# Optimization experiments

Measured on AMD Instinct MI355X. Metric: run time of the kernel, lower is better.

Reference implementation:

```python
import jax, jax.numpy as jnp
import numpy as np

N = 100000      # nodes
E = 1600000     # edges
H = 128         # hidden_channels
G = 128         # graphs in batch
L = 3           # num_layers
C = 4           # num_classes
BN_EPS = 1e-5


def setup_inputs() -> dict:
    key = jax.random.key(0)
    ks = jax.random.split(key, 24)
    s = 0.05
    x = jax.random.randint(ks[0], (N, 3), 0, 5, dtype=jnp.int64)
    edge_index = jax.random.randint(ks[1], (2, E), 0, N, dtype=jnp.int64)
    batch = jnp.sort(jax.random.randint(ks[2], (N,), 0, G, dtype=jnp.int64))
    p = lambda k, shp: jax.random.normal(k, shp, dtype=jnp.float32) * s
    return {
        'x': x, 'edge_index': edge_index, 'batch': batch,
        'node_emb': p(ks[3], (5, H)),
        'comp_emb': p(ks[4], (6, H)),
        'pin_emb':  p(ks[5], (6, H)),
        'proj_w': p(ks[6], (3 * H, H)), 'proj_b': p(ks[7], (H,)),
        'gin_w1': p(ks[8], (L, H, 2 * H)), 'gin_b1': p(ks[9], (L, 2 * H)),
        'gin_w2': p(ks[10], (L, 2 * H, H)), 'gin_b2': p(ks[11], (L, H)),
        'bn_gamma': jnp.ones((L, H), jnp.float32),
        'bn_beta': jnp.zeros((L, H), jnp.float32),
        'fus_w1': p(ks[12], (3 * H, 2 * H)), 'fus_b1': p(ks[13], (2 * H,)),
        'fus_w2': p(ks[14], (2 * H, H)), 'fus_b2': p(ks[15], (H,)),
        'cls_w': p(ks[16], (H, C)), 'cls_b': p(ks[17], (C,)),
    }


def _encoder(x, edge_index, batch, node_emb, comp_emb, pin_emb, proj_w, proj_b,
             gin_w1, gin_b1, gin_w2, gin_b2, bn_gamma, bn_beta):
    # embedding concat + projection
    idx = jnp.clip(x, 0, None)
    h = jnp.concatenate([node_emb[idx[:, 0]], comp_emb[idx[:, 1]], pin_emb[idx[:, 2]]], axis=1)
    h = h @ proj_w + proj_b                      # [N, H]
    src, dst = edge_index[0], edge_index[1]
    for i in range(L):
        # GINConv (eps=0): MLP(x + sum_{j->i} x_j)
        agg = jax.ops.segment_sum(h[src], dst, num_segments=N)
        z = h + agg
        z = jax.nn.relu(z @ gin_w1[i] + gin_b1[i]) @ gin_w2[i] + gin_b2[i]
        # BatchNorm1d (training-mode batch statistics), ReLU, residual
        mu = jnp.mean(z, axis=0)
        var = jnp.mean((z - mu) ** 2, axis=0)
        z = (z - mu) * jax.lax.rsqrt(var + BN_EPS) * bn_gamma[i] + bn_beta[i]
        z = jax.nn.relu(z)
        if i > 0:
            z = z + h
        h = z  # dropout = identity (eval)
    # global mean / max / sum pooling
    counts = jax.ops.segment_sum(jnp.ones((N,), h.dtype), batch, num_segments=G)
    gsum = jax.ops.segment_sum(h, batch, num_segments=G)
    gmean = gsum / jnp.maximum(counts, 1.0)[:, None]
    gmax = jax.ops.segment_max(h, batch, num_segments=G)
    gmax = jnp.where(jnp.isfinite(gmax), gmax, 0.0)
    return jnp.concatenate([gmean, gmax, gsum], axis=1)  # [G, 3H]


def reference(x, edge_index, batch, node_emb, comp_emb, pin_emb, proj_w, proj_b,
              gin_w1, gin_b1, gin_w2, gin_b2, bn_gamma, bn_beta,
              fus_w1, fus_b1, fus_w2, fus_b2, cls_w, cls_b):
    emb = _encoder(x, edge_index, batch, node_emb, comp_emb, pin_emb, proj_w, proj_b,
                   gin_w1, gin_b1, gin_w2, gin_b2, bn_gamma, bn_beta)
    f = jax.nn.relu(emb @ fus_w1 + fus_b1)
    f = jax.nn.relu(f @ fus_w2 + fus_b2)
    return f @ cls_w + cls_b                     # [G, C] logits
```

## Files before the change

kernel.cpp:

```cpp
#include <hip/hip_runtime.h>
#include <hip/hip_bf16.h>


#define NN 100000
#define NE 1600000
#define HD 128
#define NG 128
#define NL 3
#define BN_EPS 1e-5f
#define MPAD 100096
#define PCH 8

typedef unsigned short u16;
typedef __attribute__((ext_vector_type(8))) short short8v;
typedef __attribute__((ext_vector_type(4))) float f32x4;

__device__ inline u16 bf16_hi(float v) {
    __hip_bfloat16 h = __float2bfloat16(v);
    return *(u16*)&h;
}
__device__ inline float bf16_f(u16 u) {
    __hip_bfloat16 h = *(__hip_bfloat16*)&u;
    return __bfloat162float(h);
}
__device__ inline void split_bf16(float v, u16* hi, u16* lo) {
    u16 h = bf16_hi(v);
    *hi = h;
    *lo = bf16_hi(v - bf16_f(h));
}

__device__ inline void gload_lds16(const void* g, void* l) {
    __builtin_amdgcn_global_load_lds(
        (const __attribute__((address_space(1))) void*)g,
        (__attribute__((address_space(3))) void*)l, 16, 0, 0);
}

__global__ void proj_tables_kernel(const float* __restrict__ node_emb,
                                   const float* __restrict__ comp_emb,
                                   const float* __restrict__ pin_emb,
                                   const float* __restrict__ proj_w,
                                   float* __restrict__ P) {
    int c = threadIdx.x;
    for (int r = 0; r < 17; ++r) {
        const float* emb;
        int base;
        if (r < 5)        { emb = node_emb + r * HD;        base = 0; }
        else if (r < 11)  { emb = comp_emb + (r - 5) * HD;  base = HD; }
        else              { emb = pin_emb + (r - 11) * HD;  base = 2 * HD; }
        float acc = 0.f;
        for (int k = 0; k < HD; ++k)
            acc += emb[k] * proj_w[(size_t)(base + k) * HD + c];
        P[r * HD + c] = acc;
    }
}

__global__ __launch_bounds__(256) void embed_kernel(const int* __restrict__ x,
                                                    const float* __restrict__ P,
                                                    const float* __restrict__ proj_b,
                                                    float* __restrict__ h) {
    int i = blockIdx.x * 256 + threadIdx.x;
    int n = i >> 5;
    if (n >= NN) return;
    int c4 = (i & 31) * 4;
    int i0 = x[3 * n + 0]; i0 = i0 < 0 ? 0 : (i0 > 4 ? 4 : i0);
    int i1 = x[3 * n + 1]; i1 = i1 < 0 ? 0 : (i1 > 5 ? 5 : i1);
    int i2 = x[3 * n + 2]; i2 = i2 < 0 ? 0 : (i2 > 5 ? 5 : i2);
    float4 a = *(const float4*)(P + i0 * HD + c4);
    float4 b = *(const float4*)(P + (5 + i1) * HD + c4);
    float4 c = *(const float4*)(P + (11 + i2) * HD + c4);
    float4 bb = *(const float4*)(proj_b + c4);
    float4 o;
    o.x = a.x + b.x + c.x + bb.x;
    o.y = a.y + b.y + c.y + bb.y;
    o.z = a.z + b.z + c.z + bb.z;
    o.w = a.w + b.w + c.w + bb.w;
    *(float4*)(h + (size_t)n * HD + c4) = o;
}

__global__ void hist_kernel(const int* __restrict__ dst, int* __restrict__ deg,
                            int* __restrict__ rank) {
    int e = blockIdx.x * 256 + threadIdx.x;
    if (e < NE) rank[e] = atomicAdd(&deg[dst[e]], 1);
}

__global__ __launch_bounds__(256) void scan1_kernel(const int* __restrict__ deg,
                                                    int* __restrict__ rowstart,
                                                    int* __restrict__ partials) {
    __shared__ int arr[256];
    int blk = blockIdx.x, t = threadIdx.x;
    int base = blk * 2048 + t * 8;
    int v[8];
    int s = 0;
#pragma unroll
    for (int j = 0; j < 8; ++j) {
        int idx = base + j;
        int d = (idx < NN) ? deg[idx] : 0;
        v[j] = s;
        s += d;
    }
    int own = s;
    arr[t] = s;
    __syncthreads();
    for (int off = 1; off < 256; off <<= 1) {
        int add = (t >= off) ? arr[t - off] : 0;
        __syncthreads();
        arr[t] += add;
        __syncthreads();
    }
    int excl = arr[t] - own;
#pragma unroll
    for (int j = 0; j < 8; ++j) {
        int idx = base + j;
        if (idx < NN) rowstart[idx] = excl + v[j];
    }
    if (t == 255) partials[blk] = arr[255];
}

__global__ void scan2_kernel(int* __restrict__ partials, int* __restrict__ rowstart, int nblk) {
    if (threadIdx.x == 0) {
        int run = 0;
        for (int b = 0; b < nblk; ++b) {
            int p = partials[b];
            partials[b] = run;
            run += p;
        }
        rowstart[NN] = run;
    }
}

__global__ void scan3_kernel(int* __restrict__ rowstart, const int* __restrict__ partials) {
    int i = blockIdx.x * 256 + threadIdx.x;
    if (i < NN) rowstart[i] += partials[i >> 11];
}

__global__ void fill_kernel(const int* __restrict__ src, const int* __restrict__ dst,
                            const int* __restrict__ rowstart, const int* __restrict__ rank,
                            int* __restrict__ csr_src) {
    int e = blockIdx.x * 256 + threadIdx.x;
    if (e < NE) csr_src[rowstart[dst[e]] + rank[e]] = src[e];
}

__global__ __launch_bounds__(256) void segsum_kernel(const float* __restrict__ h,
                                                     const int* __restrict__ rowstart,
                                                     const int* __restrict__ csr_src,
                                                     u16* __restrict__ zhi,
                                                     u16* __restrict__ zlo) {
    int wid = (blockIdx.x * 256 + threadIdx.x) >> 6;
    int lane = threadIdx.x & 63;
    if (wid >= NN) return;
    int beg = __builtin_amdgcn_readfirstlane(rowstart[wid]);
    int end = __builtin_amdgcn_readfirstlane(rowstart[wid + 1]);
    const float2* hp = (const float2*)h;
    float2 acc = hp[(size_t)wid * 64 + lane];
    for (int base = beg; base < end; base += 64) {
        int cnt = end - base;
        if (cnt > 64) cnt = 64;
        int idx = (lane < cnt) ? csr_src[base + lane] : 0;
        int j = 0;
        for (; j + 8 <= cnt; j += 8) {
            int s0 = __shfl(idx, j);
            int s1 = __shfl(idx, j + 1);
            int s2 = __shfl(idx, j + 2);
            int s3 = __shfl(idx, j + 3);
            int s4 = __shfl(idx, j + 4);
            int s5 = __shfl(idx, j + 5);
            int s6 = __shfl(idx, j + 6);
            int s7 = __shfl(idx, j + 7);
            float2 v0 = hp[(size_t)s0 * 64 + lane];
            float2 v1 = hp[(size_t)s1 * 64 + lane];
            float2 v2 = hp[(size_t)s2 * 64 + lane];
            float2 v3 = hp[(size_t)s3 * 64 + lane];
            float2 v4 = hp[(size_t)s4 * 64 + lane];
            float2 v5 = hp[(size_t)s5 * 64 + lane];
            float2 v6 = hp[(size_t)s6 * 64 + lane];
            float2 v7 = hp[(size_t)s7 * 64 + lane];
            acc.x += v0.x; acc.y += v0.y;
            acc.x += v1.x; acc.y += v1.y;
            acc.x += v2.x; acc.y += v2.y;
            acc.x += v3.x; acc.y += v3.y;
            acc.x += v4.x; acc.y += v4.y;
            acc.x += v5.x; acc.y += v5.y;
            acc.x += v6.x; acc.y += v6.y;
            acc.x += v7.x; acc.y += v7.y;
        }
        for (; j < cnt; ++j) {
            int s = __shfl(idx, j);
            float2 v = hp[(size_t)s * 64 + lane];
            acc.x += v.x;
            acc.y += v.y;
        }
    }
    u16 h0, l0, h1, l1;
    split_bf16(acc.x, &h0, &l0);
    split_bf16(acc.y, &h1, &l1);
    ushort2 vh; vh.x = h0; vh.y = h1;
    ushort2 vl; vl.x = l0; vl.y = l1;
    ((ushort2*)zhi)[(size_t)wid * 64 + lane] = vh;
    ((ushort2*)zlo)[(size_t)wid * 64 + lane] = vl;
}

__global__ __launch_bounds__(256) void prep_weights_kernel(const float* __restrict__ gw1,
                                                           const float* __restrict__ gw2,
                                                           u16* __restrict__ w1hi, u16* __restrict__ w1lo,
                                                           u16* __restrict__ w2hi, u16* __restrict__ w2lo) {
    int i = blockIdx.x * 256 + threadIdx.x;
    if (i >= NL * 32768) return;
    int l = i / 32768, rem = i % 32768;
    int n1 = rem >> 7, k1 = rem & 127;
    split_bf16(gw1[(size_t)l * 32768 + (size_t)k1 * 256 + n1], &w1hi[i], &w1lo[i]);
    int n2 = rem >> 8, k2 = rem & 255;
    split_bf16(gw2[(size_t)l * 32768 + (size_t)k2 * 128 + n2], &w2hi[i], &w2lo[i]);
}

template <int K, int N, int RELU, int SPLIT, int STATS>
__global__ __launch_bounds__(256) void gemm_sp(const u16* __restrict__ Ahi, const u16* __restrict__ Alo,
                                               const u16* __restrict__ Bhi, const u16* __restrict__ Blo,
                                               const float* __restrict__ bias,
                                               u16* __restrict__ Ohi, u16* __restrict__ Olo,
                                               float* __restrict__ Of,
                                               float* __restrict__ sums) {
    __shared__ __align__(16) u16 lds[16384];
    const int t = threadIdx.x;
    const int wv = t >> 6, lane = t & 63;
    const int l15 = lane & 15, l4 = lane >> 4;
    const int m0 = blockIdx.x * 128, n0 = blockIdx.y * 128;
    const int wm = wv >> 1, wn = wv & 1;
    const int lrow = lane >> 2, lchunk = lane & 3;

    f32x4 acc[4][4];
#pragma unroll
    for (int m = 0; m < 4; ++m)
#pragma unroll
        for (int n = 0; n < 4; ++n)
            acc[m][n] = (f32x4){0.f, 0.f, 0.f, 0.f};

    for (int kb = 0; kb < K; kb += 32) {
#pragma unroll
        for (int p = 0; p < 4; ++p) {
            const u16* plane = (p == 0) ? Ahi : (p == 1) ? Alo : (p == 2) ? Bhi : Blo;
            const int rbase = (p < 2) ? m0 : n0;
#pragma unroll
            for (int hh = 0; hh < 2; ++hh) {
                int row = hh * 64 + wv * 16 + lrow;
                int cg = lchunk ^ ((row >> 1) & 3);
                const u16* src = plane + (size_t)(rbase + row) * K + kb + cg * 8;
                u16* dst = lds + p * 4096 + hh * 2048 + wv * 512;
                gload_lds16(src, dst);
            }
        }
        __syncthreads();

        short8v ah[4], al[4], bh[4], bl[4];
#pragma unroll
        for (int i = 0; i < 4; ++i) {
            int rowA = wm * 64 + i * 16 + l15;
            int pca = l4 ^ ((rowA >> 1) & 3);
            ah[i] = *(const short8v*)(lds + 0    + rowA * 32 + pca * 8);
            al[i] = *(const short8v*)(lds + 4096 + rowA * 32 + pca * 8);
            int rowB = wn * 64 + i * 16 + l15;
            int pcb = l4 ^ ((rowB >> 1) & 3);
            bh[i] = *(const short8v*)(lds + 8192  + rowB * 32 + pcb * 8);
            bl[i] = *(const short8v*)(lds + 12288 + rowB * 32 + pcb * 8);
        }
#pragma unroll
        for (int m = 0; m < 4; ++m)
#pragma unroll
            for (int n = 0; n < 4; ++n) {
                acc[m][n] = __builtin_amdgcn_mfma_f32_16x16x32_bf16(ah[m], bh[n], acc[m][n], 0, 0, 0);
                acc[m][n] = __builtin_amdgcn_mfma_f32_16x16x32_bf16(ah[m], bl[n], acc[m][n], 0, 0, 0);
                acc[m][n] = __builtin_amdgcn_mfma_f32_16x16x32_bf16(al[m], bh[n], acc[m][n], 0, 0, 0);
            }
        __syncthreads();
    }

#pragma unroll
    for (int n = 0; n < 4; ++n) {
        int gcol = n0 + wn * 64 + n * 16 + l15;
        float bv = bias[gcol];
        float s = 0.f, q = 0.f;
#pragma unroll
        for (int m = 0; m < 4; ++m) {
#pragma unroll
            for (int r = 0; r < 4; ++r) {
                int grow = m0 + wm * 64 + m * 16 + l4 * 4 + r;
                float v = acc[m][n][r] + bv;
                if (RELU) v = fmaxf(v, 0.f);
                if (SPLIT) {
                    u16 hi, lo;
                    split_bf16(v, &hi, &lo);
                    Ohi[(size_t)grow * N + gcol] = hi;
                    Olo[(size_t)grow * N + gcol] = lo;
                } else {
                    Of[(size_t)grow * N + gcol] = v;
                }
                if (STATS) {
                    if (grow < NN) { s += v; q += v * v; }
                }
            }
        }
        if (STATS) {
            s += __shfl_xor(s, 16); s += __shfl_xor(s, 32);
            q += __shfl_xor(q, 16); q += __shfl_xor(q, 32);
            if (l4 == 0) {
                atomicAdd(&sums[gcol], s);
                atomicAdd(&sums[128 + gcol], q);
            }
        }
    }
}

__global__ void bn_finalize_kernel(const float* __restrict__ sums,
                                   const float* __restrict__ gamma,
                                   const float* __restrict__ beta,
                                   float* __restrict__ scale, float* __restrict__ shift) {
    int c = threadIdx.x;
    float mean = sums[c] / (float)NN;
    float var = sums[128 + c] / (float)NN - mean * mean;
    float rstd = rsqrtf(fmaxf(var, 0.f) + BN_EPS);
    float sc = rstd * gamma[c];
    scale[c] = sc;
    shift[c] = beta[c] - mean * sc;
}

__global__ __launch_bounds__(256) void bn_apply_kernel(const float* __restrict__ z2,
                                                       const float* __restrict__ scale,
                                                       const float* __restrict__ shift,
                                                       float* __restrict__ h, int use_res) {
    int i = blockIdx.x * 256 + threadIdx.x;
    if (i >= NN * 32) return;
    int c4 = (i & 31) * 4;
    float4 v = ((const float4*)z2)[i];
    float4 sc = *(const float4*)(scale + c4);
    float4 sh = *(const float4*)(shift + c4);
    float4 o;
    o.x = fmaxf(v.x * sc.x + sh.x, 0.f);
    o.y = fmaxf(v.y * sc.y + sh.y, 0.f);
    o.z = fmaxf(v.z * sc.z + sh.z, 0.f);
    o.w = fmaxf(v.w * sc.w + sh.w, 0.f);
    if (use_res) {
        float4 r = ((float4*)h)[i];
        o.x += r.x; o.y += r.y; o.z += r.z; o.w += r.w;
    }
    ((float4*)h)[i] = o;
}

__global__ __launch_bounds__(256) void pool_part_kernel(const float* __restrict__ h,
                                                        const int* __restrict__ batch,
                                                        float* __restrict__ psum,
                                                        float* __restrict__ pmax) {
    __shared__ int bounds[2];
    __shared__ float redS[256], redM[256];
    int g = blockIdx.x, chunk = blockIdx.y, t = threadIdx.x;
    if (t < 2) {
        int target = g + t, lo = 0, hi = NN;
        while (lo < hi) {
            int mid = (lo + hi) >> 1;
            if (batch[mid] < target) lo = mid + 1;
            else hi = mid;
        }
        bounds[t] = lo;
    }
    __syncthreads();
    int lo = bounds[0], hi = bounds[1], len = hi - lo;
    int c0 = lo + (len * chunk) / PCH;
    int c1 = lo + (len * (chunk + 1)) / PCH;
    int c = t & 127, half = t >> 7;
    float s = 0.f, m = -3.4e38f;
    for (int r = c0 + half; r < c1; r += 2) {
        float v = h[(size_t)r * HD + c];
        s += v;
        m = fmaxf(m, v);
    }
    redS[t] = s;
    redM[t] = m;
    __syncthreads();
    if (t < 128) {
        psum[((size_t)g * PCH + chunk) * HD + t] = redS[t] + redS[t + 128];
        pmax[((size_t)g * PCH + chunk) * HD + t] = fmaxf(redM[t], redM[t + 128]);
    }
}

__global__ __launch_bounds__(128) void pool_combine_kernel(const float* __restrict__ psum,
                                                           const float* __restrict__ pmax,
                                                           const int* __restrict__ batch,
                                                           float* __restrict__ emb) {
    __shared__ int bounds[2];
    int g = blockIdx.x, t = threadIdx.x;
    if (t < 2) {
        int target = g + t, lo = 0, hi = NN;
        while (lo < hi) {
            int mid = (lo + hi) >> 1;
            if (batch[mid] < target) lo = mid + 1;
            else hi = mid;
        }
        bounds[t] = lo;
    }
    __syncthreads();
    int len = bounds[1] - bounds[0];
    float s = 0.f, m = -3.4e38f;
#pragma unroll
    for (int ch = 0; ch < PCH; ++ch) {
        s += psum[((size_t)g * PCH + ch) * HD + t];
        m = fmaxf(m, pmax[((size_t)g * PCH + ch) * HD + t]);
    }
    float mean;
    if (len > 0) {
        mean = s / (float)len;
    } else {
        mean = 0.f; m = 0.f; s = 0.f;
    }
    emb[g * 384 + t] = mean;
    emb[g * 384 + 128 + t] = m;
    emb[g * 384 + 256 + t] = s;
}

__global__ __launch_bounds__(256) void head_kernel(const float* __restrict__ emb,
                                                   const float* __restrict__ w1, const float* __restrict__ b1,
                                                   const float* __restrict__ w2, const float* __restrict__ b2,
                                                   const float* __restrict__ cw, const float* __restrict__ cb,
                                                   float* __restrict__ out) {
    __shared__ float e[384], f1[256], f2[128];
    int g = blockIdx.x, t = threadIdx.x;
    e[t] = emb[g * 384 + t];
    if (t < 128) e[256 + t] = emb[g * 384 + 256 + t];
    __syncthreads();
    float acc = b1[t];
    for (int k = 0; k < 384; ++k) acc += e[k] * w1[(size_t)k * 256 + t];
    f1[t] = fmaxf(acc, 0.f);
    __syncthreads();
    if (t < 128) {
        float a2 = b2[t];
        for (int k = 0; k < 256; ++k) a2 += f1[k] * w2[k * 128 + t];
        f2[t] = fmaxf(a2, 0.f);
    }
    __syncthreads();
    if (t < 4) {
        float a3 = cb[t];
        for (int k = 0; k < 128; ++k) a3 += f2[k] * cw[k * 4 + t];
        out[g * 4 + t] = a3;
    }
}

extern "C" void kernel_launch(void* const* d_in, const int* in_sizes, int n_in,
                              void* d_out, int out_size, void* d_ws, size_t ws_size,
                              hipStream_t stream) {
    const int* x = (const int*)d_in[0];
    const int* edge = (const int*)d_in[1];
    const int* batch = (const int*)d_in[2];
    const float* node_emb = (const float*)d_in[3];
    const float* comp_emb = (const float*)d_in[4];
    const float* pin_emb = (const float*)d_in[5];
    const float* proj_w = (const float*)d_in[6];
    const float* proj_b = (const float*)d_in[7];
    const float* gin_w1 = (const float*)d_in[8];
    const float* gin_b1 = (const float*)d_in[9];
    const float* gin_w2 = (const float*)d_in[10];
    const float* gin_b2 = (const float*)d_in[11];
    const float* bn_gamma = (const float*)d_in[12];
    const float* bn_beta = (const float*)d_in[13];
    const float* fus_w1 = (const float*)d_in[14];
    const float* fus_b1 = (const float*)d_in[15];
    const float* fus_w2 = (const float*)d_in[16];
    const float* fus_b2 = (const float*)d_in[17];
    const float* cls_w = (const float*)d_in[18];
    const float* cls_b = (const float*)d_in[19];

    const int* esrc = edge;
    const int* edst = edge + NE;

    char* ws = (char*)d_ws;
    size_t off = 0;
    auto alloc = [&](size_t bytes) -> void* {
        void* p = ws + off;
        off = (off + bytes + 255) & ~(size_t)255;
        return p;
    };
    float* h = (float*)alloc((size_t)NN * HD * 4);
    char* zu = (char*)alloc((size_t)MPAD * HD * 4);
    u16* z_hi = (u16*)zu;
    u16* z_lo = z_hi + (size_t)MPAD * HD;
    float* z2 = (float*)zu;
    u16* z1_hi = (u16*)alloc((size_t)MPAD * 256 * 2);
    u16* z1_lo = (u16*)alloc((size_t)MPAD * 256 * 2);
    u16* w1hi = (u16*)alloc((size_t)NL * 32768 * 2);
    u16* w1lo = (u16*)alloc((size_t)NL * 32768 * 2);
    u16* w2hi = (u16*)alloc((size_t)NL * 32768 * 2);
    u16* w2lo = (u16*)alloc((size_t)NL * 32768 * 2);
    float* P = (float*)alloc(17 * HD * 4);
    float* sums = (float*)alloc(256 * 4);
    float* scale = (float*)alloc(HD * 4);
    float* shift = (float*)alloc(HD * 4);
    float* emb = (float*)alloc((size_t)NG * 384 * 4);
    float* psum = (float*)alloc((size_t)NG * PCH * HD * 4);
    float* pmax = (float*)alloc((size_t)NG * PCH * HD * 4);
    int* deg = (int*)alloc((size_t)NN * 4);
    int* rowstart = (int*)alloc((size_t)(NN + 1) * 4);
    int* rank = (int*)alloc((size_t)NE * 4);
    int* csr_src = (int*)alloc((size_t)NE * 4);
    int* partials = (int*)alloc(64 * 4);

    proj_tables_kernel<<<1, 128, 0, stream>>>(node_emb, comp_emb, pin_emb, proj_w, P);
    embed_kernel<<<(NN * 32 + 255) / 256, 256, 0, stream>>>(x, P, proj_b, h);
    prep_weights_kernel<<<(NL * 32768 + 255) / 256, 256, 0, stream>>>(gin_w1, gin_w2,
                                                                      w1hi, w1lo, w2hi, w2lo);

    hipMemsetAsync(deg, 0, (size_t)NN * 4, stream);
    hist_kernel<<<(NE + 255) / 256, 256, 0, stream>>>(edst, deg, rank);
    int nblk = (NN + 2047) / 2048;
    scan1_kernel<<<nblk, 256, 0, stream>>>(deg, rowstart, partials);
    scan2_kernel<<<1, 64, 0, stream>>>(partials, rowstart, nblk);
    scan3_kernel<<<(NN + 255) / 256, 256, 0, stream>>>(rowstart, partials);
    fill_kernel<<<(NE + 255) / 256, 256, 0, stream>>>(esrc, edst, rowstart, rank, csr_src);

    const int gm = MPAD / 128;
    for (int l = 0; l < NL; ++l) {
        segsum_kernel<<<(NN * 64 + 255) / 256, 256, 0, stream>>>(h, rowstart, csr_src, z_hi, z_lo);
        gemm_sp<128, 256, 1, 1, 0><<<dim3(gm, 2), 256, 0, stream>>>(
            z_hi, z_lo, w1hi + (size_t)l * 32768, w1lo + (size_t)l * 32768,
            gin_b1 + (size_t)l * 256, z1_hi, z1_lo, nullptr, nullptr);
        hipMemsetAsync(sums, 0, 256 * 4, stream);
        gemm_sp<256, 128, 0, 0, 1><<<dim3(gm, 1), 256, 0, stream>>>(
            z1_hi, z1_lo, w2hi + (size_t)l * 32768, w2lo + (size_t)l * 32768,
            gin_b2 + (size_t)l * HD, nullptr, nullptr, z2, sums);
        bn_finalize_kernel<<<1, 128, 0, stream>>>(sums, bn_gamma + l * HD, bn_beta + l * HD, scale, shift);
        bn_apply_kernel<<<(NN * 32 + 255) / 256, 256, 0, stream>>>(z2, scale, shift, h, l > 0 ? 1 : 0);
    }

    pool_part_kernel<<<dim3(NG, PCH), 256, 0, stream>>>(h, batch, psum, pmax);
    pool_combine_kernel<<<NG, 128, 0, stream>>>(psum, pmax, batch, emb);
    head_kernel<<<NG, 256, 0, stream>>>(emb, fus_w1, fus_b1, fus_w2, fus_b2, cls_w, cls_b,
                                        (float*)d_out);
}
```

Baseline: 1.110 ms.

## Fuse neighbor aggregation into first GIN GEMM via LDS staging

Replaces the separate segment-sum kernel and first GIN GEMM with one kernel per 128-row tile. Eight waves gather and sum neighbor rows, write the split bf16 hi/lo result into swizzled LDS, then run MFMA against the full 256-wide W1 with B fragments read straight from global memory. This removes the round trip of the aggregated z through global memory and one kernel launch. In exchange, the gather runs with only 782 blocks of 512 threads, so there is less parallelism to hide gather latency, and load imbalance between rows can stall the GEMM phase inside a block.

```diff
diff --git a/kernel.cpp b/kernel.cpp
--- a/kernel.cpp
+++ b/kernel.cpp
@@ -12,6 +12,7 @@
 #define PCH 8
 
 typedef unsigned short u16;
+typedef unsigned int u32;
 typedef __attribute__((ext_vector_type(8))) short short8v;
 typedef __attribute__((ext_vector_type(4))) float f32x4;
 
@@ -140,65 +141,6 @@
     if (e < NE) csr_src[rowstart[dst[e]] + rank[e]] = src[e];
 }
 
-__global__ __launch_bounds__(256) void segsum_kernel(const float* __restrict__ h,
-                                                     const int* __restrict__ rowstart,
-                                                     const int* __restrict__ csr_src,
-                                                     u16* __restrict__ zhi,
-                                                     u16* __restrict__ zlo) {
-    int wid = (blockIdx.x * 256 + threadIdx.x) >> 6;
-    int lane = threadIdx.x & 63;
-    if (wid >= NN) return;
-    int beg = __builtin_amdgcn_readfirstlane(rowstart[wid]);
-    int end = __builtin_amdgcn_readfirstlane(rowstart[wid + 1]);
-    const float2* hp = (const float2*)h;
-    float2 acc = hp[(size_t)wid * 64 + lane];
-    for (int base = beg; base < end; base += 64) {
-        int cnt = end - base;
-        if (cnt > 64) cnt = 64;
-        int idx = (lane < cnt) ? csr_src[base + lane] : 0;
-        int j = 0;
-        for (; j + 8 <= cnt; j += 8) {
-            int s0 = __shfl(idx, j);
-            int s1 = __shfl(idx, j + 1);
-            int s2 = __shfl(idx, j + 2);
-            int s3 = __shfl(idx, j + 3);
-            int s4 = __shfl(idx, j + 4);
-            int s5 = __shfl(idx, j + 5);
-            int s6 = __shfl(idx, j + 6);
-            int s7 = __shfl(idx, j + 7);
-            float2 v0 = hp[(size_t)s0 * 64 + lane];
-            float2 v1 = hp[(size_t)s1 * 64 + lane];
-            float2 v2 = hp[(size_t)s2 * 64 + lane];
-            float2 v3 = hp[(size_t)s3 * 64 + lane];
-            float2 v4 = hp[(size_t)s4 * 64 + lane];
-            float2 v5 = hp[(size_t)s5 * 64 + lane];
-            float2 v6 = hp[(size_t)s6 * 64 + lane];
-            float2 v7 = hp[(size_t)s7 * 64 + lane];
-            acc.x += v0.x; acc.y += v0.y;
-            acc.x += v1.x; acc.y += v1.y;
-            acc.x += v2.x; acc.y += v2.y;
-            acc.x += v3.x; acc.y += v3.y;
-            acc.x += v4.x; acc.y += v4.y;
-            acc.x += v5.x; acc.y += v5.y;
-            acc.x += v6.x; acc.y += v6.y;
-            acc.x += v7.x; acc.y += v7.y;
-        }
-        for (; j < cnt; ++j) {
-            int s = __shfl(idx, j);
-            float2 v = hp[(size_t)s * 64 + lane];
-            acc.x += v.x;
-            acc.y += v.y;
-        }
-    }
-    u16 h0, l0, h1, l1;
-    split_bf16(acc.x, &h0, &l0);
-    split_bf16(acc.y, &h1, &l1);
-    ushort2 vh; vh.x = h0; vh.y = h1;
-    ushort2 vl; vl.x = l0; vl.y = l1;
-    ((ushort2*)zhi)[(size_t)wid * 64 + lane] = vh;
-    ((ushort2*)zlo)[(size_t)wid * 64 + lane] = vl;
-}
-
 __global__ __launch_bounds__(256) void prep_weights_kernel(const float* __restrict__ gw1,
                                                            const float* __restrict__ gw2,
                                                            u16* __restrict__ w1hi, u16* __restrict__ w1lo,
@@ -210,6 +152,138 @@
     split_bf16(gw1[(size_t)l * 32768 + (size_t)k1 * 256 + n1], &w1hi[i], &w1lo[i]);
     int n2 = rem >> 8, k2 = rem & 255;
     split_bf16(gw2[(size_t)l * 32768 + (size_t)k2 * 128 + n2], &w2hi[i], &w2lo[i]);
+}
+
+__global__ __launch_bounds__(512, 4) void gin1_fused(const float* __restrict__ h,
+                                                     const int* __restrict__ rowstart,
+                                                     const int* __restrict__ csr_src,
+                                                     const u16* __restrict__ Bhi,
+                                                     const u16* __restrict__ Blo,
+                                                     const float* __restrict__ bias,
+                                                     u16* __restrict__ Ohi,
+                                                     u16* __restrict__ Olo) {
+    __shared__ __align__(16) u16 zh[16384];
+    __shared__ __align__(16) u16 zl[16384];
+    const int t = threadIdx.x;
+    const int wv = t >> 6, lane = t & 63;
+    const int m0 = blockIdx.x * 128;
+
+    const float2* hp = (const float2*)h;
+    for (int i = 0; i < 16; ++i) {
+        int lr = wv * 16 + i;
+        int gr = m0 + lr;
+        int hrow = gr < NN ? gr : NN - 1;
+        float2 acc = hp[(size_t)hrow * 64 + lane];
+        int beg = 0, end = 0;
+        if (gr < NN) {
+            beg = __builtin_amdgcn_readfirstlane(rowstart[gr]);
+            end = __builtin_amdgcn_readfirstlane(rowstart[gr + 1]);
+        }
+        for (int base = beg; base < end; base += 64) {
+            int cnt = end - base;
+            if (cnt > 64) cnt = 64;
+            int idx = (lane < cnt) ? csr_src[base + lane] : 0;
+            int j = 0;
+            for (; j + 8 <= cnt; j += 8) {
+                int s0 = __shfl(idx, j);
+                int s1 = __shfl(idx, j + 1);
+                int s2 = __shfl(idx, j + 2);
+                int s3 = __shfl(idx, j + 3);
+                int s4 = __shfl(idx, j + 4);
+                int s5 = __shfl(idx, j + 5);
+                int s6 = __shfl(idx, j + 6);
+                int s7 = __shfl(idx, j + 7);
+                float2 v0 = hp[(size_t)s0 * 64 + lane];
+                float2 v1 = hp[(size_t)s1 * 64 + lane];
+                float2 v2 = hp[(size_t)s2 * 64 + lane];
+                float2 v3 = hp[(size_t)s3 * 64 + lane];
+                float2 v4 = hp[(size_t)s4 * 64 + lane];
+                float2 v5 = hp[(size_t)s5 * 64 + lane];
+                float2 v6 = hp[(size_t)s6 * 64 + lane];
+                float2 v7 = hp[(size_t)s7 * 64 + lane];
+                acc.x += v0.x; acc.y += v0.y;
+                acc.x += v1.x; acc.y += v1.y;
+                acc.x += v2.x; acc.y += v2.y;
+                acc.x += v3.x; acc.y += v3.y;
+                acc.x += v4.x; acc.y += v4.y;
+                acc.x += v5.x; acc.y += v5.y;
+                acc.x += v6.x; acc.y += v6.y;
+                acc.x += v7.x; acc.y += v7.y;
+            }
+            for (; j < cnt; ++j) {
+                int s = __shfl(idx, j);
+                float2 v = hp[(size_t)s * 64 + lane];
+                acc.x += v.x;
+                acc.y += v.y;
+            }
+        }
+        u16 h0, l0, h1, l1;
+        split_bf16(acc.x, &h0, &l0);
+        split_bf16(acc.y, &h1, &l1);
+        int addr = lr * 128 + (((lane >> 2) ^ (lr & 7)) << 3) + (lane & 3) * 2;
+        *(u32*)(zh + addr) = (u32)h0 | ((u32)h1 << 16);
+        *(u32*)(zl + addr) = (u32)l0 | ((u32)l1 << 16);
+    }
+    __syncthreads();
+
+    const int wm = wv >> 2, wn = wv & 3;
+    const int l15 = lane & 15, l4 = lane >> 4;
+    f32x4 acc[4][4];
+#pragma unroll
+    for (int m = 0; m < 4; ++m)
+#pragma unroll
+        for (int n = 0; n < 4; ++n)
+            acc[m][n] = (f32x4){0.f, 0.f, 0.f, 0.f};
+
+#pragma unroll
+    for (int ks = 0; ks < 4; ++ks) {
+        short8v ah[4], al[4];
+#pragma unroll
+        for (int m = 0; m < 4; ++m) {
+            int rA = wm * 64 + m * 16 + l15;
+            int au = rA * 128 + (((ks * 4 + l4) ^ (rA & 7)) << 3);
+            ah[m] = *(const short8v*)(zh + au);
+            al[m] = *(const short8v*)(zl + au);
+        }
+        int col0 = wn * 64 + l15;
+        const u16* bph = Bhi + (size_t)col0 * 128 + ks * 32 + l4 * 8;
+        const u16* bpl = Blo + (size_t)col0 * 128 + ks * 32 + l4 * 8;
+        short8v bh_cur = *(const short8v*)bph;
+        short8v bl_cur = *(const short8v*)bpl;
+#pragma unroll
+        for (int n = 0; n < 4; ++n) {
+            short8v bh_nxt, bl_nxt;
+            if (n < 3) {
+                bh_nxt = *(const short8v*)(bph + (n + 1) * 16 * 128);
+                bl_nxt = *(const short8v*)(bpl + (n + 1) * 16 * 128);
+            }
+#pragma unroll
+            for (int m = 0; m < 4; ++m) {
+                acc[m][n] = __builtin_amdgcn_mfma_f32_16x16x32_bf16(ah[m], bh_cur, acc[m][n], 0, 0, 0);
+                acc[m][n] = __builtin_amdgcn_mfma_f32_16x16x32_bf16(ah[m], bl_cur, acc[m][n], 0, 0, 0);
+                acc[m][n] = __builtin_amdgcn_mfma_f32_16x16x32_bf16(al[m], bh_cur, acc[m][n], 0, 0, 0);
+            }
+            if (n < 3) { bh_cur = bh_nxt; bl_cur = bl_nxt; }
+        }
+    }
+
+#pragma unroll
+    for (int n = 0; n < 4; ++n) {
+        int gcol = wn * 64 + n * 16 + l15;
+        float bv = bias[gcol];
+#pragma unroll
+        for (int m = 0; m < 4; ++m) {
+#pragma unroll
+            for (int r = 0; r < 4; ++r) {
+                int grow = m0 + wm * 64 + m * 16 + l4 * 4 + r;
+                float v = fmaxf(acc[m][n][r] + bv, 0.f);
+                u16 hi, lo;
+                split_bf16(v, &hi, &lo);
+                Ohi[(size_t)grow * 256 + gcol] = hi;
+                Olo[(size_t)grow * 256 + gcol] = lo;
+            }
+        }
+    }
 }
 
 template <int K, int N, int RELU, int SPLIT, int STATS>
@@ -476,10 +550,7 @@
         return p;
     };
     float* h = (float*)alloc((size_t)NN * HD * 4);
-    char* zu = (char*)alloc((size_t)MPAD * HD * 4);
-    u16* z_hi = (u16*)zu;
-    u16* z_lo = z_hi + (size_t)MPAD * HD;
-    float* z2 = (float*)zu;
+    float* z2 = (float*)alloc((size_t)MPAD * HD * 4);
     u16* z1_hi = (u16*)alloc((size_t)MPAD * 256 * 2);
     u16* z1_lo = (u16*)alloc((size_t)MPAD * 256 * 2);
     u16* w1hi = (u16*)alloc((size_t)NL * 32768 * 2);
@@ -514,10 +585,9 @@
 
     const int gm = MPAD / 128;
     for (int l = 0; l < NL; ++l) {
-        segsum_kernel<<<(NN * 64 + 255) / 256, 256, 0, stream>>>(h, rowstart, csr_src, z_hi, z_lo);
-        gemm_sp<128, 256, 1, 1, 0><<<dim3(gm, 2), 256, 0, stream>>>(
-            z_hi, z_lo, w1hi + (size_t)l * 32768, w1lo + (size_t)l * 32768,
-            gin_b1 + (size_t)l * 256, z1_hi, z1_lo, nullptr, nullptr);
+        gin1_fused<<<gm, 512, 0, stream>>>(h, rowstart, csr_src,
+                                           w1hi + (size_t)l * 32768, w1lo + (size_t)l * 32768,
+                                           gin_b1 + (size_t)l * 256, z1_hi, z1_lo);
         hipMemsetAsync(sums, 0, 256 * 4, stream);
         gemm_sp<256, 128, 0, 0, 1><<<dim3(gm, 1), 256, 0, stream>>>(
             z1_hi, z1_lo, w2hi + (size_t)l * 32768, w2lo + (size_t)l * 32768,
```

New measurement: 1.234 ms. +11.2%, slower.

## Fuse GIN MLP's two GEMMs into one kernel keeping hidden layer in LDS

Applied to the files above, without the earlier changes.

Replaces the two split-bf16 GEMM launches per layer with one kernel that processes 64-row tiles. Each tile's 256-wide hidden activation is computed in two halves, staged in LDS with an XOR swizzle, and consumed at once by the second GEMM, which also gathers the batch-norm statistics. This removes the round trip through global memory for the hi/lo hidden planes (about 100 MB per layer). In exchange, weight fragments are now read straight from global or L2 rather than staged in LDS, and the 64 KB of LDS per block may limit occupancy.

```diff
diff --git a/kernel.cpp b/kernel.cpp
--- a/kernel.cpp
+++ b/kernel.cpp
@@ -12,6 +12,7 @@
 #define PCH 8
 
 typedef unsigned short u16;
+typedef unsigned int u32;
 typedef __attribute__((ext_vector_type(8))) short short8v;
 typedef __attribute__((ext_vector_type(4))) float f32x4;
 
@@ -212,99 +213,134 @@
     split_bf16(gw2[(size_t)l * 32768 + (size_t)k2 * 128 + n2], &w2hi[i], &w2lo[i]);
 }
 
-template <int K, int N, int RELU, int SPLIT, int STATS>
-__global__ __launch_bounds__(256) void gemm_sp(const u16* __restrict__ Ahi, const u16* __restrict__ Alo,
-                                               const u16* __restrict__ Bhi, const u16* __restrict__ Blo,
-                                               const float* __restrict__ bias,
-                                               u16* __restrict__ Ohi, u16* __restrict__ Olo,
-                                               float* __restrict__ Of,
-                                               float* __restrict__ sums) {
-    __shared__ __align__(16) u16 lds[16384];
+__global__ __launch_bounds__(256) void gin_mlp(const u16* __restrict__ zH, const u16* __restrict__ zL,
+                                               const u16* __restrict__ W1h, const u16* __restrict__ W1l,
+                                               const u16* __restrict__ W2h, const u16* __restrict__ W2l,
+                                               const float* __restrict__ b1, const float* __restrict__ b2,
+                                               float* __restrict__ Of, float* __restrict__ sums) {
+    __shared__ __align__(16) u16 zh[8192], zl[8192];
+    __shared__ __align__(16) u16 z1h[8192], z1l[8192];
     const int t = threadIdx.x;
     const int wv = t >> 6, lane = t & 63;
     const int l15 = lane & 15, l4 = lane >> 4;
-    const int m0 = blockIdx.x * 128, n0 = blockIdx.y * 128;
-    const int wm = wv >> 1, wn = wv & 1;
-    const int lrow = lane >> 2, lchunk = lane & 3;
-
-    f32x4 acc[4][4];
+    const int m0 = blockIdx.x * 64;
+
+    {
+        int rlo = lane >> 4;
+        int cpos = lane & 15;
+        for (int i = 0; i < 4; ++i) {
+            int lrow = wv * 16 + i * 4 + rlo;
+            int sc = cpos ^ (lrow & 15);
+            gload_lds16(zH + (size_t)(m0 + lrow) * 128 + sc * 8, zh + wv * 2048 + i * 512);
+            gload_lds16(zL + (size_t)(m0 + lrow) * 128 + sc * 8, zl + wv * 2048 + i * 512);
+        }
+    }
+    __syncthreads();
+
+    f32x4 a2[4][2];
 #pragma unroll
     for (int m = 0; m < 4; ++m)
 #pragma unroll
-        for (int n = 0; n < 4; ++n)
-            acc[m][n] = (f32x4){0.f, 0.f, 0.f, 0.f};
-
-    for (int kb = 0; kb < K; kb += 32) {
-#pragma unroll
-        for (int p = 0; p < 4; ++p) {
-            const u16* plane = (p == 0) ? Ahi : (p == 1) ? Alo : (p == 2) ? Bhi : Blo;
-            const int rbase = (p < 2) ? m0 : n0;
-#pragma unroll
-            for (int hh = 0; hh < 2; ++hh) {
-                int row = hh * 64 + wv * 16 + lrow;
-                int cg = lchunk ^ ((row >> 1) & 3);
-                const u16* src = plane + (size_t)(rbase + row) * K + kb + cg * 8;
-                u16* dst = lds + p * 4096 + hh * 2048 + wv * 512;
-                gload_lds16(src, dst);
+        for (int n = 0; n < 2; ++n)
+            a2[m][n] = (f32x4){0.f, 0.f, 0.f, 0.f};
+
+    for (int half = 0; half < 2; ++half) {
+        f32x4 a1[4][2];
+#pragma unroll
+        for (int m = 0; m < 4; ++m)
+#pragma unroll
+            for (int n = 0; n < 2; ++n)
+                a1[m][n] = (f32x4){0.f, 0.f, 0.f, 0.f};
+
+#pragma unroll
+        for (int ks = 0; ks < 4; ++ks) {
+            short8v ah[4], al[4];
+#pragma unroll
+            for (int m = 0; m < 4; ++m) {
+                int rA = m * 16 + l15;
+                int au = rA * 128 + (((ks * 4 + l4) ^ (rA & 15)) << 3);
+                ah[m] = *(const short8v*)(zh + au);
+                al[m] = *(const short8v*)(zl + au);
             }
+#pragma unroll
+            for (int n = 0; n < 2; ++n) {
+                int col = half * 128 + wv * 32 + n * 16 + l15;
+                short8v bh = *(const short8v*)(W1h + (size_t)col * 128 + ks * 32 + l4 * 8);
+                short8v bl = *(const short8v*)(W1l + (size_t)col * 128 + ks * 32 + l4 * 8);
+#pragma unroll
+                for (int m = 0; m < 4; ++m) {
+                    a1[m][n] = __builtin_amdgcn_mfma_f32_16x16x32_bf16(ah[m], bh, a1[m][n], 0, 0, 0);
+                    a1[m][n] = __builtin_amdgcn_mfma_f32_16x16x32_bf16(ah[m], bl, a1[m][n], 0, 0, 0);
+                    a1[m][n] = __builtin_amdgcn_mfma_f32_16x16x32_bf16(al[m], bh, a1[m][n], 0, 0, 0);
+                }
+            }
         }
         __syncthreads();
-
-        short8v ah[4], al[4], bh[4], bl[4];
-#pragma unroll
-        for (int i = 0; i < 4; ++i) {
-            int rowA = wm * 64 + i * 16 + l15;
-            int pca = l4 ^ ((rowA >> 1) & 3);
-            ah[i] = *(const short8v*)(lds + 0    + rowA * 32 + pca * 8);
-            al[i] = *(const short8v*)(lds + 4096 + rowA * 32 + pca * 8);
-            int rowB = wn * 64 + i * 16 + l15;
-            int pcb = l4 ^ ((rowB >> 1) & 3);
-            bh[i] = *(const short8v*)(lds + 8192  + rowB * 32 + pcb * 8);
-            bl[i] = *(const short8v*)(lds + 12288 + rowB * 32 + pcb * 8);
-        }
-#pragma unroll
-        for (int m = 0; m < 4; ++m)
-#pragma unroll
-            for (int n = 0; n < 4; ++n) {
-                acc[m][n] = __builtin_amdgcn_mfma_f32_16x16x32_bf16(ah[m], bh[n], acc[m][n], 0, 0, 0);
-                acc[m][n] = __builtin_amdgcn_mfma_f32_16x16x32_bf16(ah[m], bl[n], acc[m][n], 0, 0, 0);
-                acc[m][n] = __builtin_amdgcn_mfma_f32_16x16x32_bf16(al[m], bh[n], acc[m][n], 0, 0, 0);
-            }
-        __syncthreads();
-    }
-
-#pragma unroll
-    for (int n = 0; n < 4; ++n) {
-        int gcol = n0 + wn * 64 + n * 16 + l15;
-        float bv = bias[gcol];
-        float s = 0.f, q = 0.f;
-#pragma unroll
-        for (int m = 0; m < 4; ++m) {
-#pragma unroll
-            for (int r = 0; r < 4; ++r) {
-                int grow = m0 + wm * 64 + m * 16 + l4 * 4 + r;
-                float v = acc[m][n][r] + bv;
-                if (RELU) v = fmaxf(v, 0.f);
-                if (SPLIT) {
+#pragma unroll
+        for (int n = 0; n < 2; ++n) {
+            int colL = wv * 32 + n * 16 + l15;
+            float bv = b1[half * 128 + colL];
+#pragma unroll
+            for (int m = 0; m < 4; ++m) {
+#pragma unroll
+                for (int r = 0; r < 4; ++r) {
+                    int row = m * 16 + l4 * 4 + r;
+                    float v = fmaxf(a1[m][n][r] + bv, 0.f);
                     u16 hi, lo;
                     split_bf16(v, &hi, &lo);
-                    Ohi[(size_t)grow * N + gcol] = hi;
-                    Olo[(size_t)grow * N + gcol] = lo;
-                } else {
-                    Of[(size_t)grow * N + gcol] = v;
-                }
-                if (STATS) {
-                    if (grow < NN) { s += v; q += v * v; }
+                    int addr = row * 128 + (((colL >> 3) ^ (row & 15)) << 3) + (colL & 7);
+                    z1h[addr] = hi;
+                    z1l[addr] = lo;
                 }
             }
         }
-        if (STATS) {
-            s += __shfl_xor(s, 16); s += __shfl_xor(s, 32);
-            q += __shfl_xor(q, 16); q += __shfl_xor(q, 32);
-            if (l4 == 0) {
-                atomicAdd(&sums[gcol], s);
-                atomicAdd(&sums[128 + gcol], q);
+        __syncthreads();
+#pragma unroll
+        for (int ks = 0; ks < 4; ++ks) {
+            short8v ah[4], al[4];
+#pragma unroll
+            for (int m = 0; m < 4; ++m) {
+                int rA = m * 16 + l15;
+                int au = rA * 128 + (((ks * 4 + l4) ^ (rA & 15)) << 3);
+                ah[m] = *(const short8v*)(z1h + au);
+                al[m] = *(const short8v*)(z1l + au);
             }
+#pragma unroll
+            for (int n = 0; n < 2; ++n) {
+                int col = wv * 32 + n * 16 + l15;
+                int kk = half * 128 + ks * 32 + l4 * 8;
+                short8v bh = *(const short8v*)(W2h + (size_t)col * 256 + kk);
+                short8v bl = *(const short8v*)(W2l + (size_t)col * 256 + kk);
+#pragma unroll
+                for (int m = 0; m < 4; ++m) {
+                    a2[m][n] = __builtin_amdgcn_mfma_f32_16x16x32_bf16(ah[m], bh, a2[m][n], 0, 0, 0);
+                    a2[m][n] = __builtin_amdgcn_mfma_f32_16x16x32_bf16(ah[m], bl, a2[m][n], 0, 0, 0);
+                    a2[m][n] = __builtin_amdgcn_mfma_f32_16x16x32_bf16(al[m], bh, a2[m][n], 0, 0, 0);
+                }
+            }
+        }
+    }
+
+#pragma unroll
+    for (int n = 0; n < 2; ++n) {
+        int gcol = wv * 32 + n * 16 + l15;
+        float bv = b2[gcol];
+        float s = 0.f, q = 0.f;
+#pragma unroll
+        for (int m = 0; m < 4; ++m) {
+#pragma unroll
+            for (int r = 0; r < 4; ++r) {
+                int grow = m0 + m * 16 + l4 * 4 + r;
+                float v = a2[m][n][r] + bv;
+                Of[(size_t)grow * HD + gcol] = v;
+                if (grow < NN) { s += v; q += v * v; }
+            }
+        }
+        s += __shfl_xor(s, 16); s += __shfl_xor(s, 32);
+        q += __shfl_xor(q, 16); q += __shfl_xor(q, 32);
+        if (l4 == 0) {
+            atomicAdd(&sums[gcol], s);
+            atomicAdd(&sums[128 + gcol], q);
         }
     }
 }
@@ -476,12 +512,9 @@
         return p;
     };
     float* h = (float*)alloc((size_t)NN * HD * 4);
-    char* zu = (char*)alloc((size_t)MPAD * HD * 4);
-    u16* z_hi = (u16*)zu;
-    u16* z_lo = z_hi + (size_t)MPAD * HD;
-    float* z2 = (float*)zu;
-    u16* z1_hi = (u16*)alloc((size_t)MPAD * 256 * 2);
-    u16* z1_lo = (u16*)alloc((size_t)MPAD * 256 * 2);
+    u16* z_hi = (u16*)alloc((size_t)MPAD * HD * 2);
+    u16* z_lo = (u16*)alloc((size_t)MPAD * HD * 2);
+    float* z2 = (float*)alloc((size_t)MPAD * HD * 4);
     u16* w1hi = (u16*)alloc((size_t)NL * 32768 * 2);
     u16* w1lo = (u16*)alloc((size_t)NL * 32768 * 2);
     u16* w2hi = (u16*)alloc((size_t)NL * 32768 * 2);
@@ -512,16 +545,15 @@
     scan3_kernel<<<(NN + 255) / 256, 256, 0, stream>>>(rowstart, partials);
     fill_kernel<<<(NE + 255) / 256, 256, 0, stream>>>(esrc, edst, rowstart, rank, csr_src);
 
-    const int gm = MPAD / 128;
+    const int gm = MPAD / 64;
     for (int l = 0; l < NL; ++l) {
         segsum_kernel<<<(NN * 64 + 255) / 256, 256, 0, stream>>>(h, rowstart, csr_src, z_hi, z_lo);
-        gemm_sp<128, 256, 1, 1, 0><<<dim3(gm, 2), 256, 0, stream>>>(
-            z_hi, z_lo, w1hi + (size_t)l * 32768, w1lo + (size_t)l * 32768,
-            gin_b1 + (size_t)l * 256, z1_hi, z1_lo, nullptr, nullptr);
         hipMemsetAsync(sums, 0, 256 * 4, stream);
-        gemm_sp<256, 128, 0, 0, 1><<<dim3(gm, 1), 256, 0, stream>>>(
-            z1_hi, z1_lo, w2hi + (size_t)l * 32768, w2lo + (size_t)l * 32768,
-            gin_b2 + (size_t)l * HD, nullptr, nullptr, z2, sums);
+        gin_mlp<<<gm, 256, 0, stream>>>(z_hi, z_lo,
+                                        w1hi + (size_t)l * 32768, w1lo + (size_t)l * 32768,
+                                        w2hi + (size_t)l * 32768, w2lo + (size_t)l * 32768,
+                                        gin_b1 + (size_t)l * 256, gin_b2 + (size_t)l * HD,
+                                        z2, sums);
         bn_finalize_kernel<<<1, 128, 0, stream>>>(sums, bn_gamma + l * HD, bn_beta + l * HD, scale, shift);
         bn_apply_kernel<<<(NN * 32 + 255) / 256, 256, 0, stream>>>(z2, scale, shift, h, l > 0 ? 1 : 0);
     }
```

Result: faster. 1.038 ms (-6.5%).
